# Optimization experiments

Hardware: AMD Instinct MI355X
Metric: run time of the kernel (lower is better)

The kernel has to match this reference:

```python
import jax, jax.numpy as jnp
import numpy as np

N_NODES = 100000
N_EDGES = 1600000
HIDDEN = 128
SLOPE = 0.2


def setup_inputs() -> dict:
    key = jax.random.key(0)
    k1, k2, k3, k4, k5, k6 = jax.random.split(key, 6)
    x = jax.random.normal(k1, (N_NODES, HIDDEN), dtype=jnp.float32)
    W_l = jax.random.normal(k2, (HIDDEN, HIDDEN), dtype=jnp.float32) * (1.0 / np.sqrt(HIDDEN))
    W_r = jax.random.normal(k3, (HIDDEN, HIDDEN), dtype=jnp.float32) * (1.0 / np.sqrt(HIDDEN))
    alpha = jax.random.uniform(k4, (N_EDGES, 1), dtype=jnp.float32)
    src = jax.random.randint(k5, (N_EDGES,), 0, N_NODES, dtype=jnp.int32)
    dst = jax.random.randint(k6, (N_EDGES,), 0, N_NODES, dtype=jnp.int32)
    return {"x": x, "W_l": W_l, "W_r": W_r, "alpha": alpha, "src": src, "dst": dst}


def reference(x, W_l, W_r, alpha, src, dst):
    # x: [N, D]; W_l, W_r: [D, D] (nn.Linear weight layout, y = x @ W.T)
    # src, dst: [E] edge endpoints; alpha: [E, 1] scalar edge weights.
    n_nodes = x.shape[0]
    hl_all = x @ W_l.T                     # [N, D]
    hr_all = x @ W_r.T                     # [N, D]
    h_l = hl_all[src]                      # [E, D] gather by source
    h_r = hr_all[dst]                      # [E, D] gather by destination
    z = jax.nn.leaky_relu((h_l + h_r) * alpha, negative_slope=SLOPE)  # [E, D]
    e = jnp.sum(z, axis=1, keepdims=True)  # [E, 1] per-edge score
    # Destination-grouped (edge) softmax, numerically stable.
    e_max = jax.ops.segment_max(e, dst, num_segments=n_nodes)          # [N, 1]
    ex = jnp.exp(e - e_max[dst])                                       # [E, 1]
    denom = jax.ops.segment_sum(ex, dst, num_segments=n_nodes)        # [N, 1]
    a = ex / denom[dst]                                                # [E, 1]
    # Weighted scatter-sum of source features to destinations.
    msg = x[src] * a                                                   # [E, D]
    return jax.ops.segment_sum(msg, dst, num_segments=n_nodes)        # [N, D]
```

## Files before the change

kernel.cpp:

```cpp
#include <hip/hip_runtime.h>
#include <hip/hip_fp16.h>

#define HID 128
#define BCAP 16384
#define GCAP 10240

struct h8 { __half2 a, b, c, d; };

typedef _Float16 half8v __attribute__((ext_vector_type(8)));
typedef _Float16 h2v    __attribute__((ext_vector_type(2)));
typedef float floatx4  __attribute__((ext_vector_type(4)));

static __device__ __forceinline__ float fdot2h(__half2 a, __half2 b, float c) {
    h2v av, bv;
    __builtin_memcpy(&av, &a, 4);
    __builtin_memcpy(&bv, &b, 4);
    return __builtin_amdgcn_fdot2(av, bv, c, false);
}

static __device__ __forceinline__ __half2 hmax2p(__half2 a, __half2 b) {
    h2v av, bv, rv;
    __builtin_memcpy(&av, &a, 4);
    __builtin_memcpy(&bv, &b, 4);
    rv = __builtin_elementwise_max(av, bv);
    __half2 r;
    __builtin_memcpy(&r, &rv, 4);
    return r;
}

__global__ __launch_bounds__(512) void prep_kernel(
    const float* __restrict__ x, h8* __restrict__ hlx,
    const float* __restrict__ Wl, const float* __restrict__ Wr,
    __half* __restrict__ Wh,
    const int* __restrict__ dst, const int* __restrict__ src,
    const float* __restrict__ alpha, int* __restrict__ bcount,
    int2* __restrict__ bs, int nbe, int nbx, int ntot, int e)
{
    __shared__ int cnt[256], lsc[256], lbase[256], scn[256];
    __shared__ int2 sa_s[4096];
    __shared__ unsigned char bin_s[4096];

    int bid = blockIdx.x;
    int t   = threadIdx.x;

    if (bid >= nbe + nbx) {
        int i = (bid - nbe - nbx) * 4096 + t * 8;
        const float* W = (i < 16384) ? Wl : Wr;
        int ii = i & 16383;
        const float4* p = (const float4*)(W + ii);
        float4 v0 = p[0], v1 = p[1];
        h8 o;
        o.a = __float22half2_rn(make_float2(v0.x, v0.y));
        o.b = __float22half2_rn(make_float2(v0.z, v0.w));
        o.c = __float22half2_rn(make_float2(v1.x, v1.y));
        o.d = __float22half2_rn(make_float2(v1.z, v1.w));
        *(h8*)(Wh + i) = o;
        return;
    }
    if (bid >= nbe) {
        int i = (bid - nbe) * 512 + t;
        if (i < ntot) {
            const float4* p = (const float4*)x + (size_t)i * 2;
            float4 v0 = p[0], v1 = p[1];
            h8 o;
            o.a = __float22half2_rn(make_float2(v0.x, v0.y));
            o.b = __float22half2_rn(make_float2(v0.z, v0.w));
            o.c = __float22half2_rn(make_float2(v1.x, v1.y));
            o.d = __float22half2_rn(make_float2(v1.z, v1.w));
            hlx[((size_t)(i >> 4)) * 32 + 16 + (i & 15)] = o;
        }
        return;
    }

    int base = bid * 4096;
    if (t < 256) cnt[t] = 0;
    __syncthreads();

    int d[8], bn[8], lp[8];
    bool val[8];
    #pragma unroll
    for (int j = 0; j < 8; ++j) {
        int i = base + t + j * 512;
        val[j] = i < e;
        d[j]   = val[j] ? dst[i] : 0;
        bn[j]  = d[j] >> 9;
        lp[j]  = val[j] ? atomicAdd(&cnt[bn[j]], 1) : 0;
    }
    __syncthreads();

    int v = (t < 256) ? cnt[t] : 0;
    if (t < 256) scn[t] = v;
    #pragma unroll
    for (int off = 1; off < 256; off <<= 1) {
        int add = (t < 256 && t >= off) ? scn[t - off] : 0;
        __syncthreads();
        if (t < 256) scn[t] += add;
        __syncthreads();
    }
    if (t < 256) {
        lsc[t]   = scn[t] - v;
        lbase[t] = v ? atomicAdd(&bcount[t], v) : 0;
    }
    __syncthreads();

    #pragma unroll
    for (int j = 0; j < 8; ++j) {
        int i = base + t + j * 512;
        if (val[j]) {
            int pos = lsc[bn[j]] + lp[j];
            sa_s[pos]  = make_int2(src[i] | ((d[j] & 511) << 17),
                                   __float_as_int(alpha[i]));
            bin_s[pos] = (unsigned char)bn[j];
        }
    }
    __syncthreads();

    int tot = min(4096, e - base);
    for (int i = t; i < tot; i += 512) {
        int bb  = bin_s[i];
        int pos = lbase[bb] + (i - lsc[bb]);
        if (pos < BCAP) bs[(size_t)bb * BCAP + pos] = sa_s[i];
    }
}

__global__ __launch_bounds__(256) void scan2_kernel(
    const int* __restrict__ bcount, int* __restrict__ bpref,
    int* __restrict__ offs, int nbins, int n, int e)
{
    __shared__ int s[256];
    int t = threadIdx.x;
    int v = (t < nbins) ? min(bcount[t], BCAP) : 0;
    s[t] = v;
    __syncthreads();
    #pragma unroll
    for (int off = 1; off < 256; off <<= 1) {
        int add = (t >= off) ? s[t - off] : 0;
        __syncthreads();
        s[t] += add;
        __syncthreads();
    }
    if (t < nbins) bpref[t] = s[t] - v;
    if (t == 0) offs[n] = e;
}

__global__ __launch_bounds__(256) void gemm_kernel(
    __half* __restrict__ hlx_h, const __half* __restrict__ Wh,
    __half* __restrict__ hr_h, int n)
{
    int t    = threadIdx.x;
    int w    = blockIdx.x * 4 + (t >> 6);
    int mat  = (w >= 6250) ? 1 : 0;
    int rt   = w - mat * 6250;
    int row0 = rt * 16;

    int lane = t & 63;
    int fr   = lane & 15;
    int kg   = (lane >> 4) * 8;

    const __half* xrow  = hlx_h + (size_t)(row0 + fr) * 256 + 128 + kg;
    const __half* wbase = Wh + (size_t)mat * 16384 + (size_t)fr * HID + kg;

    floatx4 acc[8];
    #pragma unroll
    for (int nt = 0; nt < 8; ++nt) acc[nt] = (floatx4){0.f, 0.f, 0.f, 0.f};

    #pragma unroll
    for (int kt = 0; kt < 4; ++kt) {
        half8v a = *(const half8v*)(xrow + kt * 32);
        #pragma unroll
        for (int nt = 0; nt < 8; ++nt) {
            half8v b = *(const half8v*)(wbase + (size_t)nt * 16 * HID + kt * 32);
            acc[nt] = __builtin_amdgcn_mfma_f32_16x16x32_f16(a, b, acc[nt], 0, 0, 0);
        }
    }

    __half* H      = mat ? hr_h : hlx_h;
    int     stride = mat ? 128 : 256;
    int orow0 = row0 + (lane >> 4) * 4;
    #pragma unroll
    for (int r = 0; r < 4; ++r) {
        size_t rb = (size_t)(orow0 + r) * stride + fr;
        #pragma unroll
        for (int nt = 0; nt < 8; ++nt)
            H[rb + nt * 16] = __float2half(acc[nt][r]);
    }
}

__global__ __launch_bounds__(512) void group_kernel(
    const int2* __restrict__ bs, const int* __restrict__ bcount,
    const int* __restrict__ bpref, int* __restrict__ offs,
    int2* __restrict__ edges, int n)
{
    __shared__ int2 sal[GCAP];
    __shared__ int s[512], p[512];

    int b = blockIdx.x, t = threadIdx.x;
    int cnt  = min(bcount[b], BCAP);
    int base = bpref[b];
    const int2* mybs = bs + (size_t)b * BCAP;

    s[t] = 0;
    __syncthreads();
    for (int i = t; i < cnt; i += 512)
        atomicAdd(&s[((unsigned)mybs[i].x) >> 17], 1);
    __syncthreads();
    int v = s[t];
    #pragma unroll
    for (int off = 1; off < 512; off <<= 1) {
        int add = (t >= off) ? s[t - off] : 0;
        __syncthreads();
        s[t] += add;
        __syncthreads();
    }
    int excl = s[t] - v;
    p[t] = excl;
    int node = b * 512 + t;
    if (node < n) offs[node] = base + excl;
    __syncthreads();

    if (cnt <= GCAP) {
        for (int i = t; i < cnt; i += 512) {
            int2 r = mybs[i];
            int dl = ((unsigned)r.x) >> 17;
            r.x &= 0x1FFFF;
            int pp = atomicAdd(&p[dl], 1);
            sal[pp] = r;
        }
        __syncthreads();
        for (int i = t; i < cnt; i += 512)
            edges[base + i] = sal[i];
    } else {
        for (int i = t; i < cnt; i += 512) {
            int2 r = mybs[i];
            int dl = ((unsigned)r.x) >> 17;
            r.x &= 0x1FFFF;
            int pp = atomicAdd(&p[dl], 1);
            edges[base + pp] = r;
        }
    }
}

__global__ __launch_bounds__(256) void edge_kernel(
    const h8* __restrict__ hlx, const h8* __restrict__ hr,
    const int2* __restrict__ edges, const int* __restrict__ offs,
    float* __restrict__ out, int n, int etot)
{
    int node = blockIdx.x * 4 + (threadIdx.x >> 6);
    if (node >= n) return;
    int lane = threadIdx.x & 63;
    int sub  = lane >> 4;
    int sl   = lane & 15;

    float* orow = out + (size_t)node * HID + (sl << 3);
    int beg = offs[node];
    int end = offs[node + 1];
    end = min(end, etot);
    if (end < beg) end = beg;
    if (beg == end) {
        if (sub == 0) {
            *(float4*)orow       = make_float4(0.f, 0.f, 0.f, 0.f);
            *(float4*)(orow + 4) = make_float4(0.f, 0.f, 0.f, 0.f);
        }
        return;
    }

    h8 hv = hr[(size_t)node * 16 + sl];
    const __half2 c02 = __float2half2_rn(0.2f);
    const __half2 one2 = __float2half2_rn(1.0f);
    const float SKIP = 13.0f;
    const int smax = n - 1;

    int2 r0A, r1A, r0B, r1B;
    bool v0A, v1A, v0B, v1B;
    {
        int e0 = beg + sub, e1 = beg + 4 + sub;
        v0A = e0 < end; v1A = e1 < end;
        r0A = v0A ? edges[e0] : make_int2(0, 0);
        r1A = v1A ? edges[e1] : make_int2(0, 0);
    }

    float m = -3.0e38f, den = 0.f;
    float4 aca = make_float4(0.f, 0.f, 0.f, 0.f);
    float4 acb = make_float4(0.f, 0.f, 0.f, 0.f);

    for (int base = beg; base < end; base += 8) {
        {
            int e0 = base + 8 + sub, e1 = base + 12 + sub;
            v0B = e0 < end; v1B = e1 < end;
            r0B = v0B ? edges[e0] : make_int2(0, 0);
            r1B = v1B ? edges[e1] : make_int2(0, 0);
        }
        const h8* blk0 = hlx + (size_t)min(r0A.x, smax) * 32;
        const h8* blk1 = hlx + (size_t)min(r1A.x, smax) * 32;
        h8 hl0 = blk0[sl];
        h8 hl1 = blk1[sl];

        float S0 = 0.f, S1 = 0.f;
        __half2 z;
        z = __hadd2(hl0.a, hv.a); z = hmax2p(z, __hmul2(z, c02)); S0 = fdot2h(z, one2, S0);
        z = __hadd2(hl0.b, hv.b); z = hmax2p(z, __hmul2(z, c02)); S0 = fdot2h(z, one2, S0);
        z = __hadd2(hl0.c, hv.c); z = hmax2p(z, __hmul2(z, c02)); S0 = fdot2h(z, one2, S0);
        z = __hadd2(hl0.d, hv.d); z = hmax2p(z, __hmul2(z, c02)); S0 = fdot2h(z, one2, S0);
        z = __hadd2(hl1.a, hv.a); z = hmax2p(z, __hmul2(z, c02)); S1 = fdot2h(z, one2, S1);
        z = __hadd2(hl1.b, hv.b); z = hmax2p(z, __hmul2(z, c02)); S1 = fdot2h(z, one2, S1);
        z = __hadd2(hl1.c, hv.c); z = hmax2p(z, __hmul2(z, c02)); S1 = fdot2h(z, one2, S1);
        z = __hadd2(hl1.d, hv.d); z = hmax2p(z, __hmul2(z, c02)); S1 = fdot2h(z, one2, S1);

        S0 += __shfl_xor(S0, 1); S1 += __shfl_xor(S1, 1);
        S0 += __shfl_xor(S0, 2); S1 += __shfl_xor(S1, 2);
        S0 += __shfl_xor(S0, 4); S1 += __shfl_xor(S1, 4);
        S0 += __shfl_xor(S0, 8); S1 += __shfl_xor(S1, 8);

        float p0 = __int_as_float(r0A.y) * S0;
        float p1 = __int_as_float(r1A.y) * S1;
        if (!v0A) p0 = -3.0e38f;
        if (!v1A) p1 = -3.0e38f;

        float pm = fmaxf(p0, p1);
        pm = fmaxf(pm, __shfl_xor(pm, 16));
        pm = fmaxf(pm, __shfl_xor(pm, 32));
        if (pm > m) {
            float sc = __expf(m - pm);
            den *= sc;
            aca.x *= sc; aca.y *= sc; aca.z *= sc; aca.w *= sc;
            acb.x *= sc; acb.y *= sc; acb.z *= sc; acb.w *= sc;
            m = pm;
        }
        float w0 = __expf(p0 - m);
        float w1 = __expf(p1 - m);
        den += w0 + w1;

        if (p0 >= m - SKIP) {
            h8 x0 = blk0[16 + sl];
            float2 u;
            u = __half22float2(x0.a); aca.x = fmaf(w0, u.x, aca.x); aca.y = fmaf(w0, u.y, aca.y);
            u = __half22float2(x0.b); aca.z = fmaf(w0, u.x, aca.z); aca.w = fmaf(w0, u.y, aca.w);
            u = __half22float2(x0.c); acb.x = fmaf(w0, u.x, acb.x); acb.y = fmaf(w0, u.y, acb.y);
            u = __half22float2(x0.d); acb.z = fmaf(w0, u.x, acb.z); acb.w = fmaf(w0, u.y, acb.w);
        }
        if (p1 >= m - SKIP) {
            h8 x1 = blk1[16 + sl];
            float2 u;
            u = __half22float2(x1.a); aca.x = fmaf(w1, u.x, aca.x); aca.y = fmaf(w1, u.y, aca.y);
            u = __half22float2(x1.b); aca.z = fmaf(w1, u.x, aca.z); aca.w = fmaf(w1, u.y, aca.w);
            u = __half22float2(x1.c); acb.x = fmaf(w1, u.x, acb.x); acb.y = fmaf(w1, u.y, acb.y);
            u = __half22float2(x1.d); acb.z = fmaf(w1, u.x, acb.z); acb.w = fmaf(w1, u.y, acb.w);
        }

        r0A = r0B; r1A = r1B; v0A = v0B; v1A = v1B;
    }

    den += __shfl_xor(den, 16);
    den += __shfl_xor(den, 32);
    aca.x += __shfl_xor(aca.x, 16); aca.x += __shfl_xor(aca.x, 32);
    aca.y += __shfl_xor(aca.y, 16); aca.y += __shfl_xor(aca.y, 32);
    aca.z += __shfl_xor(aca.z, 16); aca.z += __shfl_xor(aca.z, 32);
    aca.w += __shfl_xor(aca.w, 16); aca.w += __shfl_xor(aca.w, 32);
    acb.x += __shfl_xor(acb.x, 16); acb.x += __shfl_xor(acb.x, 32);
    acb.y += __shfl_xor(acb.y, 16); acb.y += __shfl_xor(acb.y, 32);
    acb.z += __shfl_xor(acb.z, 16); acb.z += __shfl_xor(acb.z, 32);
    acb.w += __shfl_xor(acb.w, 16); acb.w += __shfl_xor(acb.w, 32);

    if (sub == 0) {
        float inv = 1.f / den;
        *(float4*)orow =
            make_float4(aca.x * inv, aca.y * inv, aca.z * inv, aca.w * inv);
        *(float4*)(orow + 4) =
            make_float4(acb.x * inv, acb.y * inv, acb.z * inv, acb.w * inv);
    }
}

extern "C" void kernel_launch(void* const* d_in, const int* in_sizes, int n_in,
                              void* d_out, int out_size, void* d_ws, size_t ws_size,
                              hipStream_t stream)
{
    const float* x     = (const float*)d_in[0];
    const float* Wl    = (const float*)d_in[1];
    const float* Wr    = (const float*)d_in[2];
    const float* alpha = (const float*)d_in[3];
    const int*   src   = (const int*)d_in[4];
    const int*   dst   = (const int*)d_in[5];
    const int n = in_sizes[0] / HID;
    const int e = in_sizes[4];
    float* out = (float*)d_out;

    const int nbins = (n + 511) / 512;

    char* ws = (char*)d_ws;
    size_t off = 0;
    auto carve = [&](size_t bytes) -> void* {
        void* p = ws + off;
        off = (off + bytes + 255) & ~(size_t)255;
        return p;
    };
    __half* hlx_h   = (__half*)carve((size_t)n * 256 * sizeof(__half));
    __half* hr_h    = (__half*)carve((size_t)n * HID * sizeof(__half));
    __half* Wh      = (__half*)carve((size_t)2 * HID * HID * sizeof(__half));
    int*    offs    = (int*)carve((size_t)(n + 1) * sizeof(int));
    int*    bcount  = (int*)carve(256 * sizeof(int));
    int*    bpref   = (int*)carve(256 * sizeof(int));
    int2*   edges   = (int2*)carve((size_t)e * sizeof(int2));
    int2*   bs      = (int2*)carve((size_t)nbins * BCAP * sizeof(int2));

    (void)hipMemsetAsync(bcount, 0, 256 * sizeof(int), stream);

    int nbe = (e + 4095) / 4096;
    int nbx = (n * 16 + 511) / 512;
    prep_kernel<<<nbe + nbx + 8, 512, 0, stream>>>(
        x, (h8*)hlx_h, Wl, Wr, Wh, dst, src, alpha, bcount, bs,
        nbe, nbx, n * 16, e);

    gemm_kernel<<<3125, 256, 0, stream>>>(hlx_h, Wh, hr_h, n);

    scan2_kernel<<<1, 256, 0, stream>>>(bcount, bpref, offs, nbins, n, e);
    group_kernel<<<nbins, 512, 0, stream>>>(bs, bcount, bpref, offs, edges, n);

    edge_kernel<<<(n + 3) / 4, 256, 0, stream>>>(
        (const h8*)hlx_h, (const h8*)hr_h, edges, offs, out, n, e);
}
```

Before: 192.2 us.

## Skip score gathers using per-node upper bounds and fold bin scan into grouping

The GEMM now also writes, per node, a scalar upper bound on that node's share of the leaky-ReLU row sum (0.6·sum + 0.4·sum|·|) for both projections. The edge kernel first picks the edge with the largest bound to seed the running max. It then skips loading and scoring a source's hl row when alpha·(U+V) falls 14 below the current max, since that edge's weight would be negligible anyway. The separate single-block scan kernel is removed, and each group block sums the preceding bin counts itself. The trade-off is an extra pass over each node's edge list plus per-edge bound loads. The skip also relies on alpha being non-negative for the bound to hold.

```diff
diff --git a/kernel.cpp b/kernel.cpp
--- a/kernel.cpp
+++ b/kernel.cpp
@@ -123,29 +123,10 @@
     }
 }
 
-__global__ __launch_bounds__(256) void scan2_kernel(
-    const int* __restrict__ bcount, int* __restrict__ bpref,
-    int* __restrict__ offs, int nbins, int n, int e)
-{
-    __shared__ int s[256];
-    int t = threadIdx.x;
-    int v = (t < nbins) ? min(bcount[t], BCAP) : 0;
-    s[t] = v;
-    __syncthreads();
-    #pragma unroll
-    for (int off = 1; off < 256; off <<= 1) {
-        int add = (t >= off) ? s[t - off] : 0;
-        __syncthreads();
-        s[t] += add;
-        __syncthreads();
-    }
-    if (t < nbins) bpref[t] = s[t] - v;
-    if (t == 0) offs[n] = e;
-}
-
 __global__ __launch_bounds__(256) void gemm_kernel(
     __half* __restrict__ hlx_h, const __half* __restrict__ Wh,
-    __half* __restrict__ hr_h, int n)
+    __half* __restrict__ hr_h, float* __restrict__ Uarr,
+    float* __restrict__ Varr, int n)
 {
     int t    = threadIdx.x;
     int w    = blockIdx.x * 4 + (t >> 6);
@@ -184,20 +165,48 @@
         for (int nt = 0; nt < 8; ++nt)
             H[rb + nt * 16] = __float2half(acc[nt][r]);
     }
+
+    float* UV = mat ? Varr : Uarr;
+    #pragma unroll
+    for (int r = 0; r < 4; ++r) {
+        float sl = 0.f, sa = 0.f;
+        #pragma unroll
+        for (int nt = 0; nt < 8; ++nt) {
+            float vv = acc[nt][r];
+            sl += vv;
+            sa += fabsf(vv);
+        }
+        sl += __shfl_xor(sl, 1); sa += __shfl_xor(sa, 1);
+        sl += __shfl_xor(sl, 2); sa += __shfl_xor(sa, 2);
+        sl += __shfl_xor(sl, 4); sa += __shfl_xor(sa, 4);
+        sl += __shfl_xor(sl, 8); sa += __shfl_xor(sa, 8);
+        if (fr == 0) UV[orow0 + r] = 0.6f * sl + 0.4f * sa;
+    }
 }
 
 __global__ __launch_bounds__(512) void group_kernel(
     const int2* __restrict__ bs, const int* __restrict__ bcount,
-    const int* __restrict__ bpref, int* __restrict__ offs,
-    int2* __restrict__ edges, int n)
+    int* __restrict__ offs, int2* __restrict__ edges, int n, int etot)
 {
     __shared__ int2 sal[GCAP];
     __shared__ int s[512], p[512];
 
     int b = blockIdx.x, t = threadIdx.x;
     int cnt  = min(bcount[b], BCAP);
-    int base = bpref[b];
     const int2* mybs = bs + (size_t)b * BCAP;
+
+    {
+        int partial = (t < b) ? min(bcount[t], BCAP) : 0;
+        s[t] = partial;
+        __syncthreads();
+        for (int off = 256; off > 0; off >>= 1) {
+            if (t < off) s[t] += s[t + off];
+            __syncthreads();
+        }
+    }
+    int base = s[0];
+    __syncthreads();
+    if (b == 0 && t == 0) offs[n] = etot;
 
     s[t] = 0;
     __syncthreads();
@@ -242,6 +251,7 @@
 
 __global__ __launch_bounds__(256) void edge_kernel(
     const h8* __restrict__ hlx, const h8* __restrict__ hr,
+    const float* __restrict__ Uarr, const float* __restrict__ Varr,
     const int2* __restrict__ edges, const int* __restrict__ offs,
     float* __restrict__ out, int n, int etot)
 {
@@ -267,8 +277,48 @@
     h8 hv = hr[(size_t)node * 16 + sl];
     const __half2 c02 = __float2half2_rn(0.2f);
     const __half2 one2 = __float2half2_rn(1.0f);
-    const float SKIP = 13.0f;
+    const float HSKIP = 14.0f;
+    const float XSKIP = 13.0f;
     const int smax = n - 1;
+    const float Vv = Varr[node];
+
+    float m;
+    {
+        float bb = -3.0e38f, ba = 0.f;
+        int bsrc = 0, bidx = 0x7FFFFFFF;
+        for (int i = beg + lane; i < end; i += 64) {
+            int2 r = edges[i];
+            int s = min(r.x, smax);
+            float al = __int_as_float(r.y);
+            float bnd = al * (Uarr[s] + Vv);
+            if (bnd > bb || (bnd == bb && i < bidx)) {
+                bb = bnd; ba = al; bsrc = s; bidx = i;
+            }
+        }
+        #pragma unroll
+        for (int k = 1; k < 64; k <<= 1) {
+            float ob = __shfl_xor(bb, k);
+            float oa = __shfl_xor(ba, k);
+            int   os = __shfl_xor(bsrc, k);
+            int   oi = __shfl_xor(bidx, k);
+            if (ob > bb || (ob == bb && oi < bidx)) {
+                bb = ob; ba = oa; bsrc = os; bidx = oi;
+            }
+        }
+        const h8* cb = hlx + (size_t)bsrc * 32;
+        h8 ch = cb[sl];
+        float S = 0.f;
+        __half2 z;
+        z = __hadd2(ch.a, hv.a); z = hmax2p(z, __hmul2(z, c02)); S = fdot2h(z, one2, S);
+        z = __hadd2(ch.b, hv.b); z = hmax2p(z, __hmul2(z, c02)); S = fdot2h(z, one2, S);
+        z = __hadd2(ch.c, hv.c); z = hmax2p(z, __hmul2(z, c02)); S = fdot2h(z, one2, S);
+        z = __hadd2(ch.d, hv.d); z = hmax2p(z, __hmul2(z, c02)); S = fdot2h(z, one2, S);
+        S += __shfl_xor(S, 1);
+        S += __shfl_xor(S, 2);
+        S += __shfl_xor(S, 4);
+        S += __shfl_xor(S, 8);
+        m = ba * S;
+    }
 
     int2 r0A, r1A, r0B, r1B;
     bool v0A, v1A, v0B, v1B;
@@ -279,7 +329,7 @@
         r1A = v1A ? edges[e1] : make_int2(0, 0);
     }
 
-    float m = -3.0e38f, den = 0.f;
+    float den = 0.f;
     float4 aca = make_float4(0.f, 0.f, 0.f, 0.f);
     float4 acb = make_float4(0.f, 0.f, 0.f, 0.f);
 
@@ -290,31 +340,45 @@
             r0B = v0B ? edges[e0] : make_int2(0, 0);
             r1B = v1B ? edges[e1] : make_int2(0, 0);
         }
-        const h8* blk0 = hlx + (size_t)min(r0A.x, smax) * 32;
-        const h8* blk1 = hlx + (size_t)min(r1A.x, smax) * 32;
-        h8 hl0 = blk0[sl];
-        h8 hl1 = blk1[sl];
-
-        float S0 = 0.f, S1 = 0.f;
-        __half2 z;
-        z = __hadd2(hl0.a, hv.a); z = hmax2p(z, __hmul2(z, c02)); S0 = fdot2h(z, one2, S0);
-        z = __hadd2(hl0.b, hv.b); z = hmax2p(z, __hmul2(z, c02)); S0 = fdot2h(z, one2, S0);
-        z = __hadd2(hl0.c, hv.c); z = hmax2p(z, __hmul2(z, c02)); S0 = fdot2h(z, one2, S0);
-        z = __hadd2(hl0.d, hv.d); z = hmax2p(z, __hmul2(z, c02)); S0 = fdot2h(z, one2, S0);
-        z = __hadd2(hl1.a, hv.a); z = hmax2p(z, __hmul2(z, c02)); S1 = fdot2h(z, one2, S1);
-        z = __hadd2(hl1.b, hv.b); z = hmax2p(z, __hmul2(z, c02)); S1 = fdot2h(z, one2, S1);
-        z = __hadd2(hl1.c, hv.c); z = hmax2p(z, __hmul2(z, c02)); S1 = fdot2h(z, one2, S1);
-        z = __hadd2(hl1.d, hv.d); z = hmax2p(z, __hmul2(z, c02)); S1 = fdot2h(z, one2, S1);
-
-        S0 += __shfl_xor(S0, 1); S1 += __shfl_xor(S1, 1);
-        S0 += __shfl_xor(S0, 2); S1 += __shfl_xor(S1, 2);
-        S0 += __shfl_xor(S0, 4); S1 += __shfl_xor(S1, 4);
-        S0 += __shfl_xor(S0, 8); S1 += __shfl_xor(S1, 8);
-
-        float p0 = __int_as_float(r0A.y) * S0;
-        float p1 = __int_as_float(r1A.y) * S1;
-        if (!v0A) p0 = -3.0e38f;
-        if (!v1A) p1 = -3.0e38f;
+        float al0 = __int_as_float(r0A.y);
+        float al1 = __int_as_float(r1A.y);
+        int s0 = min(r0A.x, smax);
+        int s1 = min(r1A.x, smax);
+        const h8* blk0 = hlx + (size_t)s0 * 32;
+        const h8* blk1 = hlx + (size_t)s1 * 32;
+
+        float bnd0 = v0A ? al0 * (Uarr[s0] + Vv) : -3.0e38f;
+        float bnd1 = v1A ? al1 * (Uarr[s1] + Vv) : -3.0e38f;
+
+        float p0 = -3.0e38f, p1 = -3.0e38f;
+        if (bnd0 >= m - HSKIP) {
+            h8 hl0 = blk0[sl];
+            float S0 = 0.f;
+            __half2 z;
+            z = __hadd2(hl0.a, hv.a); z = hmax2p(z, __hmul2(z, c02)); S0 = fdot2h(z, one2, S0);
+            z = __hadd2(hl0.b, hv.b); z = hmax2p(z, __hmul2(z, c02)); S0 = fdot2h(z, one2, S0);
+            z = __hadd2(hl0.c, hv.c); z = hmax2p(z, __hmul2(z, c02)); S0 = fdot2h(z, one2, S0);
+            z = __hadd2(hl0.d, hv.d); z = hmax2p(z, __hmul2(z, c02)); S0 = fdot2h(z, one2, S0);
+            S0 += __shfl_xor(S0, 1);
+            S0 += __shfl_xor(S0, 2);
+            S0 += __shfl_xor(S0, 4);
+            S0 += __shfl_xor(S0, 8);
+            p0 = al0 * S0;
+        }
+        if (bnd1 >= m - HSKIP) {
+            h8 hl1 = blk1[sl];
+            float S1 = 0.f;
+            __half2 z;
+            z = __hadd2(hl1.a, hv.a); z = hmax2p(z, __hmul2(z, c02)); S1 = fdot2h(z, one2, S1);
+            z = __hadd2(hl1.b, hv.b); z = hmax2p(z, __hmul2(z, c02)); S1 = fdot2h(z, one2, S1);
+            z = __hadd2(hl1.c, hv.c); z = hmax2p(z, __hmul2(z, c02)); S1 = fdot2h(z, one2, S1);
+            z = __hadd2(hl1.d, hv.d); z = hmax2p(z, __hmul2(z, c02)); S1 = fdot2h(z, one2, S1);
+            S1 += __shfl_xor(S1, 1);
+            S1 += __shfl_xor(S1, 2);
+            S1 += __shfl_xor(S1, 4);
+            S1 += __shfl_xor(S1, 8);
+            p1 = al1 * S1;
+        }
 
         float pm = fmaxf(p0, p1);
         pm = fmaxf(pm, __shfl_xor(pm, 16));
@@ -330,7 +394,7 @@
         float w1 = __expf(p1 - m);
         den += w0 + w1;
 
-        if (p0 >= m - SKIP) {
+        if (p0 >= m - XSKIP) {
             h8 x0 = blk0[16 + sl];
             float2 u;
             u = __half22float2(x0.a); aca.x = fmaf(w0, u.x, aca.x); aca.y = fmaf(w0, u.y, aca.y);
@@ -338,7 +402,7 @@
             u = __half22float2(x0.c); acb.x = fmaf(w0, u.x, acb.x); acb.y = fmaf(w0, u.y, acb.y);
             u = __half22float2(x0.d); acb.z = fmaf(w0, u.x, acb.z); acb.w = fmaf(w0, u.y, acb.w);
         }
-        if (p1 >= m - SKIP) {
+        if (p1 >= m - XSKIP) {
             h8 x1 = blk1[16 + sl];
             float2 u;
             u = __half22float2(x1.a); aca.x = fmaf(w1, u.x, aca.x); aca.y = fmaf(w1, u.y, aca.y);
@@ -396,9 +460,10 @@
     __half* hlx_h   = (__half*)carve((size_t)n * 256 * sizeof(__half));
     __half* hr_h    = (__half*)carve((size_t)n * HID * sizeof(__half));
     __half* Wh      = (__half*)carve((size_t)2 * HID * HID * sizeof(__half));
+    float*  Uarr    = (float*)carve((size_t)n * sizeof(float));
+    float*  Varr    = (float*)carve((size_t)n * sizeof(float));
     int*    offs    = (int*)carve((size_t)(n + 1) * sizeof(int));
     int*    bcount  = (int*)carve(256 * sizeof(int));
-    int*    bpref   = (int*)carve(256 * sizeof(int));
     int2*   edges   = (int2*)carve((size_t)e * sizeof(int2));
     int2*   bs      = (int2*)carve((size_t)nbins * BCAP * sizeof(int2));
 
@@ -410,11 +475,10 @@
         x, (h8*)hlx_h, Wl, Wr, Wh, dst, src, alpha, bcount, bs,
         nbe, nbx, n * 16, e);
 
-    gemm_kernel<<<3125, 256, 0, stream>>>(hlx_h, Wh, hr_h, n);
-
-    scan2_kernel<<<1, 256, 0, stream>>>(bcount, bpref, offs, nbins, n, e);
-    group_kernel<<<nbins, 512, 0, stream>>>(bs, bcount, bpref, offs, edges, n);
+    gemm_kernel<<<3125, 256, 0, stream>>>(hlx_h, Wh, hr_h, Uarr, Varr, n);
+
+    group_kernel<<<nbins, 512, 0, stream>>>(bs, bcount, offs, edges, n, e);
 
     edge_kernel<<<(n + 3) / 4, 256, 0, stream>>>(
-        (const h8*)hlx_h, (const h8*)hr_h, edges, offs, out, n, e);
-}
+        (const h8*)hlx_h, (const h8*)hr_h, Uarr, Varr, edges, offs, out, n, e);
+}
```

Result: slower. 226.9 us (+18.1%).
